# Kernel tuning notes

Hardware: AMD Instinct MI355X
Metric: run time of the kernel (lower is better)

Reference implementation:

```python
import jax, jax.numpy as jnp
import numpy as np

MARGIN = 1.0  # init kwarg
BIG = 1e9     # finite sentinel for masked reductions (dist in [0, 2])


def setup_inputs() -> dict:
    key = jax.random.key(0)
    k1, k2 = jax.random.split(key)
    embeddings = jax.random.normal(k1, (8192, 256), dtype=jnp.float32)
    labels = jax.random.randint(k2, (8192,), 0, 128)
    return {"embeddings": embeddings, "labels": labels}


def reference(embeddings, labels):
    # cosine distance matrix: 1 - x_hat @ x_hat^T, clamped at 0
    norm = jnp.linalg.norm(embeddings, axis=1, keepdims=True)
    x = embeddings / jnp.maximum(norm, 1e-12)  # matches F.normalize eps
    dist = jnp.clip(1.0 - x @ x.T, 0.0, None)  # (B, B)

    same = labels[:, None] == labels[None, :]
    eye = jnp.eye(labels.shape[0], dtype=bool)
    pos_mask = same & ~eye   # same label, different index
    neg_mask = ~same         # different label

    # hard mining: hardest positive (max dist), hardest negative (min dist)
    pos_dist = jnp.max(jnp.where(pos_mask, dist, -BIG), axis=1)  # (B,)
    neg_dist = jnp.min(jnp.where(neg_mask, dist, BIG), axis=1)   # (B,)

    valid = pos_mask.any(axis=1) & neg_mask.any(axis=1)          # (B,)
    per_anchor = jnp.maximum(pos_dist - neg_dist + MARGIN, 0.0)
    loss_sum = jnp.sum(jnp.where(valid, per_anchor, 0.0))
    count = jnp.sum(valid).astype(dist.dtype)
    return jnp.where(count > 0, loss_sum / jnp.maximum(count, 1.0), 0.0)
```

## Files before the change

kernel.cpp:

```cpp
#include <hip/hip_runtime.h>
#include <hip/hip_bf16.h>


constexpr int NB = 8192;
constexpr int ND = 256;
constexpr int BI = 256;
constexpr int BJ = 64;
constexpr int JSPLIT = 16;
constexpr int JRANGE = NB / JSPLIT;
constexpr int NITER = JRANGE / BJ;

typedef __attribute__((ext_vector_type(8))) short bf16x8;
typedef __attribute__((ext_vector_type(4))) float f32x4;

typedef __attribute__((address_space(3))) unsigned int lds_u32;
typedef __attribute__((address_space(1))) const unsigned int g_u32;

__device__ inline void load_lds16(const unsigned short* g, unsigned short* l) {
    __builtin_amdgcn_global_load_lds((g_u32*)g, (lds_u32*)l, 16, 0, 0);
}

__device__ inline unsigned short f2bf(float v) {
    __hip_bfloat16 b = __float2bfloat16(v);
    return *reinterpret_cast<unsigned short*>(&b);
}

__global__ __launch_bounds__(256) void norm_kernel(const float* __restrict__ X,
                                                   unsigned short* __restrict__ Xbt,
                                                   float* accum, int* done) {
    __shared__ float tile[32][260];
    __shared__ float psum[32][8];
    __shared__ float rscale[32];
    const int t = threadIdx.x;
    const int rb = blockIdx.x * 32;
    if (blockIdx.x == 0 && t == 0) { accum[0] = 0.f; accum[1] = 0.f; *done = 0; }
    #pragma unroll
    for (int k = 0; k < 8; k++) {
        const int f = k * 256 + t;
        const int row = f >> 6, c4 = f & 63;
        const float4 v = *((const float4*)(X + (size_t)(rb + row) * ND) + c4);
        *(float4*)&tile[row][c4 * 4] = v;
    }
    __syncthreads();
    {
        const int r = t >> 3, e = t & 7;
        float s = 0.f;
        #pragma unroll
        for (int i = 0; i < 32; i++) { const float v = tile[r][e * 32 + i]; s += v * v; }
        psum[r][e] = s;
    }
    __syncthreads();
    if (t < 32) {
        float s = 0.f;
        #pragma unroll
        for (int e = 0; e < 8; e++) s += psum[t][e];
        rscale[t] = 1.0f / fmaxf(sqrtf(s), 1e-12f);
    }
    __syncthreads();
    #pragma unroll
    for (int j = 0; j < 4; j++) {
        const int idx = j * 256 + t;
        const int q = idx >> 5, r = idx & 31;
        const float sc = rscale[r];
        unsigned short tmp[8];
        #pragma unroll
        for (int e = 0; e < 8; e++) tmp[e] = f2bf(tile[r][q * 8 + e] * sc);
        *(bf16x8*)(Xbt + ((size_t)q * NB + rb + r) * 8) = *(bf16x8*)tmp;
    }
}

__global__ __launch_bounds__(256, 2) void mine_kernel(
    const unsigned short* __restrict__ Xbt, const int* __restrict__ labels,
    float* __restrict__ posP, float* __restrict__ negP) {
    __shared__ __align__(16) unsigned short Bt[2][32 * 512];
    __shared__ float Lall[JRANGE];

    const int tid = threadIdx.x;
    const int w = tid >> 6;
    const int lane = tid & 63;
    const int quad = lane >> 4;
    const int l16 = lane & 15;

    const int rowbase = blockIdx.x * BI + w * 64;
    const int jstart = blockIdx.y * JRANGE;

    Lall[tid] = (float)labels[jstart + tid];
    Lall[256 + tid] = (float)labels[jstart + 256 + tid];

    bf16x8 afrag[4][8];
    #pragma unroll
    for (int rs = 0; rs < 4; rs++)
        #pragma unroll
        for (int kc = 0; kc < 8; kc++) {
            const size_t u = (size_t)(kc * 4 + quad) * NB + (rowbase + rs * 16 + l16);
            afrag[rs][kc] = *(const bf16x8*)(Xbt + u * 8);
        }

    float flr[4][4];
    float minK[4][4], maxK[4][4];
    #pragma unroll
    for (int rs = 0; rs < 4; rs++)
        #pragma unroll
        for (int r = 0; r < 4; r++) {
            flr[rs][r] = (float)labels[rowbase + rs * 16 + quad * 4 + r];
            minK[rs][r] = 1e30f;
            maxK[rs][r] = -1e30f;
        }

    auto stage = [&](int buf, int jt) {
        const int jbase = jstart + jt * BJ;
        #pragma unroll
        for (int s = 0; s < 8; s++) {
            const int rg = w * 8 + s;
            const int kc = rg >> 2, nfi = rg & 3;
            const size_t u = (size_t)(kc * 4 + quad) * NB + (jbase + nfi * 16 + l16);
            load_lds16(Xbt + u * 8, &Bt[buf][rg * 512]);
        }
    };

    stage(0, 0);
    __syncthreads();

    for (int jt = 0; jt < NITER; jt++) {
        const int cur = jt & 1;
        if (jt + 1 < NITER) stage(cur ^ 1, jt + 1);

        #pragma unroll
        for (int nf = 0; nf < 4; nf++) {
            const float flc = Lall[jt * BJ + nf * 16 + l16];
            f32x4 acc[4];
            #pragma unroll
            for (int rs = 0; rs < 4; rs++) acc[rs] = (f32x4){0.f, 0.f, 0.f, 0.f};
            #pragma unroll
            for (int kc = 0; kc < 8; kc++) {
                const bf16x8 b = *(const bf16x8*)(&Bt[cur][(kc * 4 + nf) * 512 + lane * 8]);
                #pragma unroll
                for (int rs = 0; rs < 4; rs++)
                    acc[rs] = __builtin_amdgcn_mfma_f32_16x16x32_bf16(
                        afrag[rs][kc], b, acc[rs], 0, 0, 0);
            }
            #pragma unroll
            for (int rs = 0; rs < 4; rs++)
                #pragma unroll
                for (int r = 0; r < 4; r++) {
                    const float d = flr[rs][r] - flc;
                    const float uu = fminf(fabsf(d), 1.0f);
                    const float key = fmaf(uu, 8.0f, acc[rs][r]);
                    minK[rs][r] = fminf(minK[rs][r], key);
                    maxK[rs][r] = fmaxf(maxK[rs][r], key);
                }
        }
        __syncthreads();
    }

    #pragma unroll
    for (int rs = 0; rs < 4; rs++)
        #pragma unroll
        for (int r = 0; r < 4; r++) {
            float p = minK[rs][r], n = maxK[rs][r];
            #pragma unroll
            for (int m = 1; m <= 8; m <<= 1) {
                p = fminf(p, __shfl_xor(p, m, 64));
                n = fmaxf(n, __shfl_xor(n, m, 64));
            }
            if (l16 == 0) {
                const int row = rowbase + rs * 16 + quad * 4 + r;
                posP[blockIdx.y * NB + row] = p;
                negP[blockIdx.y * NB + row] = n;
            }
        }
}

__global__ __launch_bounds__(256) void finish_kernel(
    const float* __restrict__ posP, const float* __restrict__ negP,
    float* accum, int* done, float* __restrict__ out) {
    const int i = blockIdx.x * 256 + threadIdx.x;
    float p = 1e30f, n = -1e30f;
    #pragma unroll
    for (int s = 0; s < JSPLIT; s++) {
        p = fminf(p, posP[s * NB + i]);
        n = fmaxf(n, negP[s * NB + i]);
    }
    const bool valid = (p < 4.0f) && (n > 4.0f);
    const float pos_d = fmaxf(1.0f - p, 0.0f);
    const float neg_d = fmaxf(1.0f - (n - 8.0f), 0.0f);
    float per = valid ? fmaxf(pos_d - neg_d + 1.0f, 0.0f) : 0.0f;
    float cnt = valid ? 1.0f : 0.0f;
    #pragma unroll
    for (int off = 32; off > 0; off >>= 1) {
        per += __shfl_down(per, off, 64);
        cnt += __shfl_down(cnt, off, 64);
    }
    __shared__ float sp[4], sc[4];
    const int wv = threadIdx.x >> 6, ln = threadIdx.x & 63;
    if (ln == 0) { sp[wv] = per; sc[wv] = cnt; }
    __syncthreads();
    if (threadIdx.x == 0) {
        atomicAdd(&accum[0], sp[0] + sp[1] + sp[2] + sp[3]);
        atomicAdd(&accum[1], sc[0] + sc[1] + sc[2] + sc[3]);
        __threadfence();
        const int old = atomicAdd(done, 1);
        if (old == (int)gridDim.x - 1) {
            const float s = __hip_atomic_load(&accum[0], __ATOMIC_RELAXED,
                                              __HIP_MEMORY_SCOPE_AGENT);
            const float c = __hip_atomic_load(&accum[1], __ATOMIC_RELAXED,
                                              __HIP_MEMORY_SCOPE_AGENT);
            out[0] = (c > 0.f) ? s / fmaxf(c, 1.f) : 0.f;
        }
    }
}

extern "C" void kernel_launch(void* const* d_in, const int* in_sizes, int n_in,
                              void* d_out, int out_size, void* d_ws, size_t ws_size,
                              hipStream_t stream) {
    const float* X = (const float*)d_in[0];
    const int* labels = (const int*)d_in[1];
    float* out = (float*)d_out;

    char* ws = (char*)d_ws;
    unsigned short* Xbt = (unsigned short*)ws;
    float* posP = (float*)(ws + (size_t)4 * 1024 * 1024);
    float* negP = posP + JSPLIT * NB;
    float* accum = negP + JSPLIT * NB;
    int* done = (int*)(accum + 2);

    norm_kernel<<<NB / 32, 256, 0, stream>>>(X, Xbt, accum, done);
    mine_kernel<<<dim3(NB / BI, JSPLIT), 256, 0, stream>>>(
        (const unsigned short*)Xbt, labels, posP, negP);
    finish_kernel<<<NB / 256, 256, 0, stream>>>(posP, negP, accum, done, out);
}
```

Before: 99.85 us.

## Double mine block rows to 512 and move norm reduction into registers

The mining kernel now runs 512 threads (8 waves) per block covering 512 anchor rows. Each staged B tile in LDS is therefore shared by twice as many rows, which halves the per-wave staging loads and the total B traffic across the grid. The grid's x dimension shrinks from 32 to 16, so there are 256 blocks, and launch_bounds(512,2) may tighten the register budget for the large afrag arrays. The norm kernel drops its LDS tile and syncs: each thread keeps 32 floats in registers and reduces row norms with shuffles.

```diff
diff --git a/kernel.cpp b/kernel.cpp
--- a/kernel.cpp
+++ b/kernel.cpp
@@ -4,7 +4,7 @@
 
 constexpr int NB = 8192;
 constexpr int ND = 256;
-constexpr int BI = 256;
+constexpr int BI = 512;
 constexpr int BJ = 64;
 constexpr int JSPLIT = 16;
 constexpr int JRANGE = NB / JSPLIT;
@@ -28,48 +28,37 @@
 __global__ __launch_bounds__(256) void norm_kernel(const float* __restrict__ X,
                                                    unsigned short* __restrict__ Xbt,
                                                    float* accum, int* done) {
-    __shared__ float tile[32][260];
-    __shared__ float psum[32][8];
-    __shared__ float rscale[32];
     const int t = threadIdx.x;
     const int rb = blockIdx.x * 32;
+    const int r = t >> 3, e = t & 7;
     if (blockIdx.x == 0 && t == 0) { accum[0] = 0.f; accum[1] = 0.f; *done = 0; }
+
+    const float4* src = (const float4*)(X + (size_t)(rb + r) * ND + e * 32);
+    float4 v[8];
+    #pragma unroll
+    for (int k = 0; k < 8; k++) v[k] = src[k];
+
+    float s = 0.f;
     #pragma unroll
     for (int k = 0; k < 8; k++) {
-        const int f = k * 256 + t;
-        const int row = f >> 6, c4 = f & 63;
-        const float4 v = *((const float4*)(X + (size_t)(rb + row) * ND) + c4);
-        *(float4*)&tile[row][c4 * 4] = v;
-    }
-    __syncthreads();
-    {
-        const int r = t >> 3, e = t & 7;
-        float s = 0.f;
-        #pragma unroll
-        for (int i = 0; i < 32; i++) { const float v = tile[r][e * 32 + i]; s += v * v; }
-        psum[r][e] = s;
-    }
-    __syncthreads();
-    if (t < 32) {
-        float s = 0.f;
-        #pragma unroll
-        for (int e = 0; e < 8; e++) s += psum[t][e];
-        rscale[t] = 1.0f / fmaxf(sqrtf(s), 1e-12f);
-    }
-    __syncthreads();
-    #pragma unroll
-    for (int j = 0; j < 4; j++) {
-        const int idx = j * 256 + t;
-        const int q = idx >> 5, r = idx & 31;
-        const float sc = rscale[r];
+        s += v[k].x * v[k].x; s += v[k].y * v[k].y;
+        s += v[k].z * v[k].z; s += v[k].w * v[k].w;
+    }
+    #pragma unroll
+    for (int m = 1; m <= 4; m <<= 1) s += __shfl_xor(s, m, 64);
+    const float sc = 1.0f / fmaxf(sqrtf(s), 1e-12f);
+
+    #pragma unroll
+    for (int k = 0; k < 4; k++) {
+        const float* f = (const float*)&v[2 * k];
         unsigned short tmp[8];
         #pragma unroll
-        for (int e = 0; e < 8; e++) tmp[e] = f2bf(tile[r][q * 8 + e] * sc);
-        *(bf16x8*)(Xbt + ((size_t)q * NB + rb + r) * 8) = *(bf16x8*)tmp;
-    }
-}
-
-__global__ __launch_bounds__(256, 2) void mine_kernel(
+        for (int q = 0; q < 8; q++) tmp[q] = f2bf(f[q] * sc);
+        *(bf16x8*)(Xbt + ((size_t)(e * 4 + k) * NB + rb + r) * 8) = *(bf16x8*)tmp;
+    }
+}
+
+__global__ __launch_bounds__(512, 2) void mine_kernel(
     const unsigned short* __restrict__ Xbt, const int* __restrict__ labels,
     float* __restrict__ posP, float* __restrict__ negP) {
     __shared__ __align__(16) unsigned short Bt[2][32 * 512];
@@ -85,7 +74,6 @@
     const int jstart = blockIdx.y * JRANGE;
 
     Lall[tid] = (float)labels[jstart + tid];
-    Lall[256 + tid] = (float)labels[jstart + 256 + tid];
 
     bf16x8 afrag[4][8];
     #pragma unroll
@@ -110,8 +98,8 @@
     auto stage = [&](int buf, int jt) {
         const int jbase = jstart + jt * BJ;
         #pragma unroll
-        for (int s = 0; s < 8; s++) {
-            const int rg = w * 8 + s;
+        for (int s = 0; s < 4; s++) {
+            const int rg = w * 4 + s;
             const int kc = rg >> 2, nfi = rg & 3;
             const size_t u = (size_t)(kc * 4 + quad) * NB + (jbase + nfi * 16 + l16);
             load_lds16(Xbt + u * 8, &Bt[buf][rg * 512]);
@@ -225,7 +213,7 @@
     int* done = (int*)(accum + 2);
 
     norm_kernel<<<NB / 32, 256, 0, stream>>>(X, Xbt, accum, done);
-    mine_kernel<<<dim3(NB / BI, JSPLIT), 256, 0, stream>>>(
+    mine_kernel<<<dim3(NB / BI, JSPLIT), 512, 0, stream>>>(
         (const unsigned short*)Xbt, labels, posP, negP);
     finish_kernel<<<NB / 256, 256, 0, stream>>>(posP, negP, accum, done, out);
 }
```

New measurement: 100.4 us. About the same (+0.6%).
